# Performance work log

Hardware: AMD Instinct MI355X
Metric: run time of the kernel (lower is better)

## Reference

```python
import jax, jax.numpy as jnp
import numpy as np


def _igd(x, pf):
    # pf: [M, d] reference front, x: [N, d] candidate set
    # squared Euclidean distances via ||a||^2 + ||b||^2 - 2 a.b (cdist expansion)
    pf_sq = jnp.sum(pf * pf, axis=1, keepdims=True)          # [M, 1]
    x_sq = jnp.sum(x * x, axis=1, keepdims=True).T            # [1, N]
    cross = pf @ x.T                                          # [M, N]
    d2 = jnp.maximum(pf_sq + x_sq - 2.0 * cross, 0.0)
    dist = jnp.sqrt(d2)                                       # [M, N]
    # IGD: mean over reference points of min distance to candidate set
    return jnp.mean(jnp.min(dist, axis=1))


def setup_inputs() -> dict:
    key = jax.random.key(0)
    k1, k2 = jax.random.split(key)
    N, M, D = 16384, 16384, 64
    x = jax.random.normal(k1, (N, D), dtype=jnp.float32)
    pf = jax.random.normal(k2, (M, D), dtype=jnp.float32)
    return {"x": x, "pf": pf}


def reference(x, pf):
    return _igd(x, pf)
```

## Files before the change

### kernel.cpp

```cpp
#include <hip/hip_runtime.h>


typedef float f32x16 __attribute__((ext_vector_type(16)));
typedef float f32x2 __attribute__((ext_vector_type(2)));
typedef int i32x8 __attribute__((ext_vector_type(8)));
typedef unsigned long long u64;

#define DIM 64
#define NSPLIT 12
#define UNITB 2048
#define CHUNKU 8
#define CHUNKB (CHUNKU * UNITB)
#define MTILE 256

union BFrag { u64 q[4]; i32x8 v; };

__device__ __forceinline__ void g2lds16(const void* g, void* l) {
    __builtin_amdgcn_global_load_lds(
        (const __attribute__((address_space(1))) unsigned int*)g,
        (__attribute__((address_space(3))) unsigned int*)l, 16, 0, 0);
}
__device__ __forceinline__ void g2lds4(const void* g, void* l) {
    __builtin_amdgcn_global_load_lds(
        (const __attribute__((address_space(1))) unsigned int*)g,
        (__attribute__((address_space(3))) unsigned int*)l, 4, 0, 0);
}

__device__ __forceinline__ void encode16(const float* f, u64 w[2], float& sumsq) {
    unsigned int w32[4];
#pragma unroll
    for (int k = 0; k < 4; ++k) {
        int lo = __builtin_amdgcn_cvt_pk_fp8_f32(f[4 * k],     f[4 * k + 1], 0,  false);
        w32[k] = __builtin_amdgcn_cvt_pk_fp8_f32(f[4 * k + 2], f[4 * k + 3], lo, true);
    }
#pragma unroll
    for (int k = 0; k < 4; ++k) {
        f32x2 d0 = __builtin_amdgcn_cvt_pk_f32_fp8(w32[k], false);
        f32x2 d1 = __builtin_amdgcn_cvt_pk_f32_fp8(w32[k], true);
        sumsq += d0.x * d0.x + d0.y * d0.y + d1.x * d1.x + d1.y * d1.y;
    }
    w[0] = (u64)w32[0] | ((u64)w32[1] << 32);
    w[1] = (u64)w32[2] | ((u64)w32[3] << 32);
}

__global__ void pack_kernel(const float* __restrict__ x, const float* __restrict__ pf,
                            unsigned char* __restrict__ Bp, unsigned char* __restrict__ Ab,
                            float* __restrict__ xsq, float* __restrict__ pfsq,
                            float* __restrict__ out, int N, int M) {
    int gid = blockIdx.x * blockDim.x + threadIdx.x;
    if (gid == 0) out[0] = 0.f;
    if (gid < N * 4) {
        int col = gid >> 2, t = gid & 3;
        const float* s = x + (size_t)col * DIM + t * 16;
        float4 v0 = *(const float4*)(s);
        float4 v1 = *(const float4*)(s + 4);
        float4 v2 = *(const float4*)(s + 8);
        float4 v3 = *(const float4*)(s + 12);
        float f[16] = {v0.x, v0.y, v0.z, v0.w, v1.x, v1.y, v1.z, v1.w,
                       v2.x, v2.y, v2.z, v2.w, v3.x, v3.y, v3.z, v3.w};
        float partial = 0.f;
        u64 w[2];
        encode16(f, w, partial);
        int u = col >> 5, c31 = col & 31;
        unsigned char* ub = Bp + (size_t)u * UNITB;
        int h = t >> 1;
#pragma unroll
        for (int ss = 0; ss < 2; ++ss) {
            int q = (t & 1) * 2 + ss;
            *(u64*)(ub + (size_t)q * 512 + (size_t)(h * 32 + c31) * 8) = w[ss];
        }
        partial += __shfl_xor(partial, 1);
        partial += __shfl_xor(partial, 2);
        if (t == 0) xsq[col] = partial;
    } else {
        int g = gid - N * 4;
        int row = g >> 2, q = g & 3;
        if (row >= M) return;
        const float* s = pf + (size_t)row * DIM + q * 16;
        float4 v0 = *(const float4*)(s);
        float4 v1 = *(const float4*)(s + 4);
        float4 v2 = *(const float4*)(s + 8);
        float4 v3 = *(const float4*)(s + 12);
        float f[16] = {v0.x, v0.y, v0.z, v0.w, v1.x, v1.y, v1.z, v1.w,
                       v2.x, v2.y, v2.z, v2.w, v3.x, v3.y, v3.z, v3.w};
#pragma unroll
        for (int j = 0; j < 16; ++j) f[j] *= -2.f;
        float partial = 0.f;
        u64 w[2];
        encode16(f, w, partial);
        *(u64*)(Ab + (size_t)row * DIM + q * 16)     = w[0];
        *(u64*)(Ab + (size_t)row * DIM + q * 16 + 8) = w[1];
        partial += __shfl_xor(partial, 1);
        partial += __shfl_xor(partial, 2);
        if (q == 0) pfsq[row] = partial * 0.25f;
    }
}

__global__ __launch_bounds__(256, 3)
void igd_main(const unsigned char* __restrict__ A, const unsigned char* __restrict__ Bp,
              const float* __restrict__ xsq, float* __restrict__ partial, int N) {
    __shared__ unsigned char ldsB[2][CHUNKB];
    __shared__ float ldsX[2][CHUNKU * 32];
    const int tid = threadIdx.x;
    const int mTile  = blockIdx.x;
    const int nsplit = blockIdx.y;
    const int lane = tid & 63;
    const int wave = tid >> 6;
    const int half = lane >> 5;
    const int l31  = lane & 31;
    const int rowBase = mTile * MTILE + wave * 64;

    const int utotal = N / 32;
    const int ubase  = utotal / NSPLIT;
    const int urem   = utotal % NSPLIT;
    const int ustart = nsplit * ubase + (nsplit < urem ? nsplit : urem);
    const int ucount = ubase + (nsplit < urem ? 1 : 0);
    const int nch = (ucount + CHUNKU - 1) / CHUNKU;

    BFrag a[2];
#pragma unroll
    for (int g = 0; g < 2; ++g) {
        const unsigned char* ap = A + (size_t)(rowBase + 32 * g + l31) * DIM + half * 32;
#pragma unroll
        for (int qq = 0; qq < 4; ++qq)
            a[g].q[qq] = *(const u64*)(ap + qq * 8);
    }

    const unsigned char* gB = Bp + (size_t)ustart * UNITB;
    const float* gX = xsq + ustart * 32;

#define STAGE(c, buf)                                                          \
    {                                                                          \
        int bytes = (ucount - (c) * CHUNKU) < CHUNKU ? (ucount - (c) * CHUNKU) * UNITB : CHUNKB; \
        const unsigned char* src = gB + (size_t)(c) * CHUNKB;                  \
        _Pragma("unroll")                                                      \
        for (int i = 0; i < 4; ++i) {                                          \
            int off = i * 4096 + tid * 16;                                     \
            if (off < bytes)                                                   \
                g2lds16(src + off, &ldsB[buf][off]);                           \
        }                                                                      \
        int xcnt = bytes >> 6;                                                 \
        if (tid < xcnt)                                                        \
            g2lds4(gX + (c) * (CHUNKU * 32) + tid, &ldsX[buf][tid]);           \
    }

    f32x16 zero, m0, m1;
#pragma unroll
    for (int r = 0; r < 16; ++r) { zero[r] = 0.f; m0[r] = 1e30f; m1[r] = 1e30f; }

#define LOADF(rr, lb, u)                                                       \
    {                                                                          \
        const unsigned char* p = (lb) + (u) * UNITB;                           \
        rr.q[0] = *(const u64*)(p);                                            \
        rr.q[1] = *(const u64*)(p + 512);                                      \
        rr.q[2] = *(const u64*)(p + 1024);                                     \
        rr.q[3] = *(const u64*)(p + 1536);                                     \
    }

#define MFMA2(accA, accB, bfrag)                                               \
    {                                                                          \
        accA = __builtin_amdgcn_mfma_scale_f32_32x32x64_f8f6f4(                \
            a[0].v, bfrag.v, zero, 0, 0, 0, 0x7F7F7F7F, 0, 0x7F7F7F7F);        \
        accB = __builtin_amdgcn_mfma_scale_f32_32x32x64_f8f6f4(                \
            a[1].v, bfrag.v, zero, 0, 0, 0, 0x7F7F7F7F, 0, 0x7F7F7F7F);        \
    }

#define MINS(accA, accB, xq)                                                   \
    {                                                                          \
        _Pragma("unroll")                                                      \
        for (int r = 0; r < 16; ++r) {                                         \
            m0[r] = fminf(m0[r], accA[r] + (xq));                              \
            m1[r] = fminf(m1[r], accB[r] + (xq));                              \
        }                                                                      \
    }

    STAGE(0, 0);
    __syncthreads();

    for (int c = 0; c < nch; ++c) {
        const int buf = c & 1;
        if (c + 1 < nch) STAGE(c + 1, buf ^ 1);
        const int cnt = (ucount - c * CHUNKU) < CHUNKU ? (ucount - c * CHUNKU) : CHUNKU;
        const unsigned char* lb = &ldsB[buf][0] + lane * 8;
        const float* lx = &ldsX[buf][0] + l31;
        if (cnt == CHUNKU) {
            BFrag b0, b1;
            LOADF(b0, lb, 0);
#pragma unroll
            for (int u = 0; u < CHUNKU; u += 2) {
                LOADF(b1, lb, u + 1);
                f32x16 acA0, acA1;
                MFMA2(acA0, acA1, b0);
                MINS(acA0, acA1, lx[u * 32]);
                if (u + 2 < CHUNKU) LOADF(b0, lb, u + 2);
                f32x16 acB0, acB1;
                MFMA2(acB0, acB1, b1);
                MINS(acB0, acB1, lx[(u + 1) * 32]);
            }
        } else {
            BFrag bt;
            for (int u = 0; u < cnt; ++u) {
                LOADF(bt, lb, u);
                f32x16 t0, t1;
                MFMA2(t0, t1, bt);
                MINS(t0, t1, lx[u * 32]);
            }
        }
        __syncthreads();
    }
#undef STAGE
#undef LOADF
#undef MFMA2
#undef MINS

#pragma unroll
    for (int mask = 1; mask <= 16; mask <<= 1) {
#pragma unroll
        for (int r = 0; r < 16; ++r) {
            m0[r] = fminf(m0[r], __shfl_xor(m0[r], mask));
            m1[r] = fminf(m1[r], __shfl_xor(m1[r], mask));
        }
    }
    if (l31 == 0) {
#pragma unroll
        for (int r = 0; r < 16; ++r) {
            int row0 = rowBase + (r & 3) + 8 * (r >> 2) + 4 * half;
            partial[(size_t)row0 * NSPLIT + nsplit] = m0[r];
            partial[(size_t)(row0 + 32) * NSPLIT + nsplit] = m1[r];
        }
    }
}

__global__ void reduce_kernel(const float* __restrict__ partial, const float* __restrict__ pfsq,
                              float* __restrict__ out, int M, float invM) {
    int row = blockIdx.x * blockDim.x + threadIdx.x;
    float v = 0.f;
    if (row < M) {
        const float* p = partial + (size_t)row * NSPLIT;
        float mn = 3.4e38f;
#pragma unroll
        for (int s = 0; s < NSPLIT; ++s) mn = fminf(mn, p[s]);
        float d2 = mn + pfsq[row];
        v = sqrtf(fmaxf(d2, 0.f)) * invM;
    }
#pragma unroll
    for (int m = 1; m < 64; m <<= 1) v += __shfl_xor(v, m);
    __shared__ float wsum[4];
    int lane = threadIdx.x & 63, w = threadIdx.x >> 6;
    if (lane == 0) wsum[w] = v;
    __syncthreads();
    if (threadIdx.x == 0) atomicAdd(out, wsum[0] + wsum[1] + wsum[2] + wsum[3]);
}

extern "C" void kernel_launch(void* const* d_in, const int* in_sizes, int n_in,
                              void* d_out, int out_size, void* d_ws, size_t ws_size,
                              hipStream_t stream) {
    const float* x  = (const float*)d_in[0];
    const float* pf = (const float*)d_in[1];
    const int N = in_sizes[0] / DIM;
    const int M = in_sizes[1] / DIM;

    char* ws = (char*)d_ws;
    unsigned char* Bp = (unsigned char*)ws;
    unsigned char* Ab = (unsigned char*)(ws + (size_t)N * DIM);
    float* xsq  = (float*)(ws + (size_t)(N + M) * DIM);
    float* pfsq = xsq + N;
    float* part = pfsq + M;

    int packThreads = (N + M) * 4;
    pack_kernel<<<dim3((packThreads + 255) / 256), 256, 0, stream>>>(
        x, pf, Bp, Ab, xsq, pfsq, (float*)d_out, N, M);
    igd_main<<<dim3(M / MTILE, NSPLIT), 256, 0, stream>>>(Ab, Bp, xsq, part, N);
    reduce_kernel<<<dim3((M + 255) / 256), 256, 0, stream>>>(part, pfsq, (float*)d_out, M, 1.f / (float)M);
}
```

Measured before the change: 87.44 us.

## Widen each wave to four 32-row groups per B fragment, drop tail handling

```diff
diff --git a/kernel.cpp b/kernel.cpp
--- a/kernel.cpp
+++ b/kernel.cpp
@@ -7,11 +7,12 @@
 typedef unsigned long long u64;
 
 #define DIM 64
-#define NSPLIT 12
+#define NSPLIT 16
 #define UNITB 2048
 #define CHUNKU 8
 #define CHUNKB (CHUNKU * UNITB)
-#define MTILE 256
+#define MTILE 512
+#define GROUPS 4
 
 union BFrag { u64 q[4]; i32x8 v; };
 
@@ -96,7 +97,7 @@
     }
 }
 
-__global__ __launch_bounds__(256, 3)
+__global__ __launch_bounds__(256, 2)
 void igd_main(const unsigned char* __restrict__ A, const unsigned char* __restrict__ Bp,
               const float* __restrict__ xsq, float* __restrict__ partial, int N) {
     __shared__ unsigned char ldsB[2][CHUNKB];
@@ -108,18 +109,16 @@
     const int wave = tid >> 6;
     const int half = lane >> 5;
     const int l31  = lane & 31;
-    const int rowBase = mTile * MTILE + wave * 64;
+    const int rowBase = mTile * MTILE + wave * (32 * GROUPS);
 
     const int utotal = N / 32;
-    const int ubase  = utotal / NSPLIT;
-    const int urem   = utotal % NSPLIT;
-    const int ustart = nsplit * ubase + (nsplit < urem ? nsplit : urem);
-    const int ucount = ubase + (nsplit < urem ? 1 : 0);
-    const int nch = (ucount + CHUNKU - 1) / CHUNKU;
-
-    BFrag a[2];
-#pragma unroll
-    for (int g = 0; g < 2; ++g) {
+    const int ucount = utotal / NSPLIT;
+    const int ustart = nsplit * ucount;
+    const int nch = ucount / CHUNKU;
+
+    BFrag a[GROUPS];
+#pragma unroll
+    for (int g = 0; g < GROUPS; ++g) {
         const unsigned char* ap = A + (size_t)(rowBase + 32 * g + l31) * DIM + half * 32;
 #pragma unroll
         for (int qq = 0; qq < 4; ++qq)
@@ -131,22 +130,23 @@
 
 #define STAGE(c, buf)                                                          \
     {                                                                          \
-        int bytes = (ucount - (c) * CHUNKU) < CHUNKU ? (ucount - (c) * CHUNKU) * UNITB : CHUNKB; \
         const unsigned char* src = gB + (size_t)(c) * CHUNKB;                  \
         _Pragma("unroll")                                                      \
         for (int i = 0; i < 4; ++i) {                                          \
             int off = i * 4096 + tid * 16;                                     \
-            if (off < bytes)                                                   \
-                g2lds16(src + off, &ldsB[buf][off]);                           \
+            g2lds16(src + off, &ldsB[buf][off]);                               \
         }                                                                      \
-        int xcnt = bytes >> 6;                                                 \
-        if (tid < xcnt)                                                        \
+        if (tid < CHUNKU * 32)                                                 \
             g2lds4(gX + (c) * (CHUNKU * 32) + tid, &ldsX[buf][tid]);           \
     }
 
-    f32x16 zero, m0, m1;
-#pragma unroll
-    for (int r = 0; r < 16; ++r) { zero[r] = 0.f; m0[r] = 1e30f; m1[r] = 1e30f; }
+    f32x16 zero, m[GROUPS];
+#pragma unroll
+    for (int r = 0; r < 16; ++r) {
+        zero[r] = 0.f;
+#pragma unroll
+        for (int g = 0; g < GROUPS; ++g) m[g][r] = 1e30f;
+    }
 
 #define LOADF(rr, lb, u)                                                       \
     {                                                                          \
@@ -157,20 +157,18 @@
         rr.q[3] = *(const u64*)(p + 1536);                                     \
     }
 
-#define MFMA2(accA, accB, bfrag)                                               \
+#define STEP4(bfrag, xq)                                                       \
     {                                                                          \
-        accA = __builtin_amdgcn_mfma_scale_f32_32x32x64_f8f6f4(                \
-            a[0].v, bfrag.v, zero, 0, 0, 0, 0x7F7F7F7F, 0, 0x7F7F7F7F);        \
-        accB = __builtin_amdgcn_mfma_scale_f32_32x32x64_f8f6f4(                \
-            a[1].v, bfrag.v, zero, 0, 0, 0, 0x7F7F7F7F, 0, 0x7F7F7F7F);        \
-    }
-
-#define MINS(accA, accB, xq)                                                   \
-    {                                                                          \
+        f32x16 acc[GROUPS];                                                    \
         _Pragma("unroll")                                                      \
-        for (int r = 0; r < 16; ++r) {                                         \
-            m0[r] = fminf(m0[r], accA[r] + (xq));                              \
-            m1[r] = fminf(m1[r], accB[r] + (xq));                              \
+        for (int g = 0; g < GROUPS; ++g)                                       \
+            acc[g] = __builtin_amdgcn_mfma_scale_f32_32x32x64_f8f6f4(          \
+                a[g].v, bfrag.v, zero, 0, 0, 0, 0x7F7F7F7F, 0, 0x7F7F7F7F);    \
+        _Pragma("unroll")                                                      \
+        for (int g = 0; g < GROUPS; ++g) {                                     \
+            _Pragma("unroll")                                                  \
+            for (int r = 0; r < 16; ++r)                                       \
+                m[g][r] = fminf(m[g][r], acc[g][r] + (xq));                    \
         }                                                                      \
     }
 
@@ -180,54 +178,39 @@
     for (int c = 0; c < nch; ++c) {
         const int buf = c & 1;
         if (c + 1 < nch) STAGE(c + 1, buf ^ 1);
-        const int cnt = (ucount - c * CHUNKU) < CHUNKU ? (ucount - c * CHUNKU) : CHUNKU;
         const unsigned char* lb = &ldsB[buf][0] + lane * 8;
         const float* lx = &ldsX[buf][0] + l31;
-        if (cnt == CHUNKU) {
-            BFrag b0, b1;
-            LOADF(b0, lb, 0);
-#pragma unroll
-            for (int u = 0; u < CHUNKU; u += 2) {
-                LOADF(b1, lb, u + 1);
-                f32x16 acA0, acA1;
-                MFMA2(acA0, acA1, b0);
-                MINS(acA0, acA1, lx[u * 32]);
-                if (u + 2 < CHUNKU) LOADF(b0, lb, u + 2);
-                f32x16 acB0, acB1;
-                MFMA2(acB0, acB1, b1);
-                MINS(acB0, acB1, lx[(u + 1) * 32]);
-            }
-        } else {
-            BFrag bt;
-            for (int u = 0; u < cnt; ++u) {
-                LOADF(bt, lb, u);
-                f32x16 t0, t1;
-                MFMA2(t0, t1, bt);
-                MINS(t0, t1, lx[u * 32]);
-            }
+        BFrag b0, b1;
+        LOADF(b0, lb, 0);
+#pragma unroll
+        for (int u = 0; u < CHUNKU; u += 2) {
+            LOADF(b1, lb, u + 1);
+            STEP4(b0, lx[u * 32]);
+            if (u + 2 < CHUNKU) LOADF(b0, lb, u + 2);
+            STEP4(b1, lx[(u + 1) * 32]);
         }
         __syncthreads();
     }
 #undef STAGE
 #undef LOADF
-#undef MFMA2
-#undef MINS
+#undef STEP4
 
 #pragma unroll
     for (int mask = 1; mask <= 16; mask <<= 1) {
 #pragma unroll
-        for (int r = 0; r < 16; ++r) {
-            m0[r] = fminf(m0[r], __shfl_xor(m0[r], mask));
-            m1[r] = fminf(m1[r], __shfl_xor(m1[r], mask));
-        }
+        for (int g = 0; g < GROUPS; ++g)
+#pragma unroll
+            for (int r = 0; r < 16; ++r)
+                m[g][r] = fminf(m[g][r], __shfl_xor(m[g][r], mask));
     }
     if (l31 == 0) {
 #pragma unroll
-        for (int r = 0; r < 16; ++r) {
-            int row0 = rowBase + (r & 3) + 8 * (r >> 2) + 4 * half;
-            partial[(size_t)row0 * NSPLIT + nsplit] = m0[r];
-            partial[(size_t)(row0 + 32) * NSPLIT + nsplit] = m1[r];
-        }
+        for (int g = 0; g < GROUPS; ++g)
+#pragma unroll
+            for (int r = 0; r < 16; ++r) {
+                int row0 = rowBase + 32 * g + (r & 3) + 8 * (r >> 2) + 4 * half;
+                partial[(size_t)row0 * NSPLIT + nsplit] = m[g][r];
+            }
     }
 }
 
```

Result: slower. 145.0 us (+65.8%).

## Fuse final reduction into main kernel via atomicMin and last-block ticket

Applied to the files above, without the earlier changes.

```diff
diff --git a/kernel.cpp b/kernel.cpp
--- a/kernel.cpp
+++ b/kernel.cpp
@@ -46,9 +46,10 @@
 __global__ void pack_kernel(const float* __restrict__ x, const float* __restrict__ pf,
                             unsigned char* __restrict__ Bp, unsigned char* __restrict__ Ab,
                             float* __restrict__ xsq, float* __restrict__ pfsq,
+                            unsigned int* __restrict__ dmin, unsigned int* __restrict__ counter,
                             float* __restrict__ out, int N, int M) {
     int gid = blockIdx.x * blockDim.x + threadIdx.x;
-    if (gid == 0) out[0] = 0.f;
+    if (gid == 0) { out[0] = 0.f; counter[0] = 0u; }
     if (gid < N * 4) {
         int col = gid >> 2, t = gid & 3;
         const float* s = x + (size_t)col * DIM + t * 16;
@@ -76,6 +77,7 @@
         int g = gid - N * 4;
         int row = g >> 2, q = g & 3;
         if (row >= M) return;
+        if (q == 1) dmin[row] = 0x7F800000u;
         const float* s = pf + (size_t)row * DIM + q * 16;
         float4 v0 = *(const float4*)(s);
         float4 v1 = *(const float4*)(s + 4);
@@ -98,7 +100,9 @@
 
 __global__ __launch_bounds__(256, 3)
 void igd_main(const unsigned char* __restrict__ A, const unsigned char* __restrict__ Bp,
-              const float* __restrict__ xsq, float* __restrict__ partial, int N) {
+              const float* __restrict__ xsq, const float* __restrict__ pfsq,
+              unsigned int* __restrict__ dmin, unsigned int* __restrict__ counter,
+              float* __restrict__ out, int N, int M) {
     __shared__ unsigned char ldsB[2][CHUNKB];
     __shared__ float ldsX[2][CHUNKU * 32];
     const int tid = threadIdx.x;
@@ -225,31 +229,35 @@
 #pragma unroll
         for (int r = 0; r < 16; ++r) {
             int row0 = rowBase + (r & 3) + 8 * (r >> 2) + 4 * half;
-            partial[(size_t)row0 * NSPLIT + nsplit] = m0[r];
-            partial[(size_t)(row0 + 32) * NSPLIT + nsplit] = m1[r];
-        }
-    }
-}
-
-__global__ void reduce_kernel(const float* __restrict__ partial, const float* __restrict__ pfsq,
-                              float* __restrict__ out, int M, float invM) {
-    int row = blockIdx.x * blockDim.x + threadIdx.x;
-    float v = 0.f;
-    if (row < M) {
-        const float* p = partial + (size_t)row * NSPLIT;
-        float mn = 3.4e38f;
-#pragma unroll
-        for (int s = 0; s < NSPLIT; ++s) mn = fminf(mn, p[s]);
-        float d2 = mn + pfsq[row];
-        v = sqrtf(fmaxf(d2, 0.f)) * invM;
-    }
-#pragma unroll
-    for (int m = 1; m < 64; m <<= 1) v += __shfl_xor(v, m);
-    __shared__ float wsum[4];
-    int lane = threadIdx.x & 63, w = threadIdx.x >> 6;
-    if (lane == 0) wsum[w] = v;
+            int row1 = row0 + 32;
+            float v0 = fmaxf(m0[r] + pfsq[row0], 0.f);
+            float v1 = fmaxf(m1[r] + pfsq[row1], 0.f);
+            atomicMin(&dmin[row0], __float_as_uint(v0));
+            atomicMin(&dmin[row1], __float_as_uint(v1));
+        }
+    }
+
+    __threadfence();
+    __shared__ int lastFlag;
+    if (tid == 0) {
+        unsigned int ticket = atomicAdd(counter, 1u);
+        lastFlag = (ticket == (unsigned int)(gridDim.x * gridDim.y - 1));
+    }
     __syncthreads();
-    if (threadIdx.x == 0) atomicAdd(out, wsum[0] + wsum[1] + wsum[2] + wsum[3]);
+    if (lastFlag) {
+        __threadfence();
+        float v = 0.f;
+        for (int i = tid; i < M; i += 256) {
+            unsigned int bits = atomicOr(&dmin[i], 0u);
+            v += sqrtf(__uint_as_float(bits));
+        }
+#pragma unroll
+        for (int mk = 1; mk < 64; mk <<= 1) v += __shfl_xor(v, mk);
+        __shared__ float wsum[4];
+        if (lane == 0) wsum[wave] = v;
+        __syncthreads();
+        if (tid == 0) out[0] = (wsum[0] + wsum[1] + wsum[2] + wsum[3]) / (float)M;
+    }
 }
 
 extern "C" void kernel_launch(void* const* d_in, const int* in_sizes, int n_in,
@@ -265,11 +273,12 @@
     unsigned char* Ab = (unsigned char*)(ws + (size_t)N * DIM);
     float* xsq  = (float*)(ws + (size_t)(N + M) * DIM);
     float* pfsq = xsq + N;
-    float* part = pfsq + M;
+    unsigned int* dmin = (unsigned int*)(pfsq + M);
+    unsigned int* counter = dmin + M;
 
     int packThreads = (N + M) * 4;
     pack_kernel<<<dim3((packThreads + 255) / 256), 256, 0, stream>>>(
-        x, pf, Bp, Ab, xsq, pfsq, (float*)d_out, N, M);
-    igd_main<<<dim3(M / MTILE, NSPLIT), 256, 0, stream>>>(Ab, Bp, xsq, part, N);
-    reduce_kernel<<<dim3((M + 255) / 256), 256, 0, stream>>>(part, pfsq, (float*)d_out, M, 1.f / (float)M);
-}
+        x, pf, Bp, Ab, xsq, pfsq, dmin, counter, (float*)d_out, N, M);
+    igd_main<<<dim3(M / MTILE, NSPLIT), 256, 0, stream>>>(
+        Ab, Bp, xsq, pfsq, dmin, counter, (float*)d_out, N, M);
+}
```

Measured after the change: 143.9 us. +64.6%, slower.
